# Kernel optimization log

Measured on AMD Instinct MI355X. Metric: run time of the kernel, lower is better.

Reference implementation:

```python
import jax, jax.numpy as jnp
import numpy as np

H_HEADS = 8
DIM_HEAD = 64


def setup_inputs() -> dict:
    key = jax.random.key(0)
    ks = jax.random.split(key, 5)
    b, c, Hs, Ws = 16, 32, 128, 128
    qd = H_HEADS * c              # 256 (heads*c = Linear in_features)
    inner = H_HEADS * DIM_HEAD    # 512
    s = 0.02                      # keep logits in a sane range
    return {
        "x": jax.random.normal(ks[0], (b, c, Hs, Ws), jnp.float32),
        "Wq": jax.random.normal(ks[1], (inner, qd), jnp.float32) * s,
        "Wkv": jax.random.normal(ks[2], (2 * inner, qd), jnp.float32) * s,
        "Wout": jax.random.normal(ks[3], (qd, inner), jnp.float32) * s,
        "bout": jax.random.normal(ks[4], (qd,), jnp.float32) * s,
    }


def _proj(arg, W, bias=None):
    # apply_operator_or_ffn for nn.Linear:
    # rearrange '(b h) n d -> b d (h n)', Linear over last dim, then 'b d n -> b n d'
    B, n, d = arg.shape
    bp = B // H_HEADS
    t = arg.reshape(bp, H_HEADS, n, d)
    t = jnp.transpose(t, (0, 3, 1, 2)).reshape(bp, d, H_HEADS * n)  # [b', d, h*n]
    y = t @ W.T
    if bias is not None:
        y = y + bias
    return jnp.transpose(y, (0, 2, 1))  # [b', out_features, d]


def _split_heads(t):
    # 'b (h d) n -> (b h) d n'
    bp, hd, n = t.shape
    return t.reshape(bp, H_HEADS, hd // H_HEADS, n).reshape(bp * H_HEADS, hd // H_HEADS, n)


def reference(x, Wq, Wkv, Wout, bout):
    b, c = x.shape[0], x.shape[1]
    spatial = x.shape[2:]
    N = int(np.prod(spatial))
    scale = DIM_HEAD ** -0.5
    xf = x.reshape(b, c, N)
    q = _proj(xf, Wq)              # [b/h, inner, N]
    kv = _proj(xf, Wkv)            # [b/h, 2*inner, N]
    inner = q.shape[1]
    k, v = kv[:, :inner], kv[:, inner:]
    qh, kh, vh = _split_heads(q), _split_heads(k), _split_heads(v)  # [b, DIM_HEAD, N]
    sim = jnp.einsum('bin,bjn->bij', qh, kh) * scale                 # [b, dh, dh]
    attn = jax.nn.softmax(sim, axis=-1)
    out = jnp.einsum('bnj,bjd->bnd', attn, vh)                       # [b, dh, N]
    out = _proj(out, Wout, bout)                                     # [b/h, h*c, N]
    return out.reshape(b, c, *spatial)
```

## Files before the change

### kernel.cpp

```cpp
#include <hip/hip_runtime.h>
#include <cstdint>
#include <cstddef>

using u16 = unsigned short;
using u32 = unsigned int;

typedef __attribute__((ext_vector_type(8))) short bf16x8;
typedef __attribute__((ext_vector_type(16))) float f32x16;

__device__ __forceinline__ u16 f2bf(float f) {
  union { float f; u32 i; } x; x.f = f;
  u32 r = (x.i + 0x7FFFu + ((x.i >> 16) & 1u)) >> 16;
  return (u16)r;
}
__device__ __forceinline__ bf16x8 ldbf16x8(const u16* p) {
  union { uint4 u; bf16x8 v; } t;
  t.u = *(const uint4*)p;
  return t.v;
}

constexpr int NP = 16384;


constexpr size_t OFF_C   = 0;
constexpr size_t OFF_T   = 131072;
constexpr size_t OFF_AT  = 393216;
constexpr size_t OFF_WE  = 458752;
constexpr size_t OFF_MT  = 720896;
constexpr size_t OFF_MA  = 851968;
constexpr size_t OFF_XB  = 917504;
constexpr size_t OFF_XBT = 5111808;
constexpr size_t OFF_CP1 = 9306112;
constexpr size_t NEED1   = (OFF_CP1 + 4194304) * 4;
constexpr size_t OFF_CP2 = 851968;
constexpr size_t NEED2   = (OFF_CP2 + 6291456) * 4;

__global__ __launch_bounds__(256)
void k0_cvt(const float* __restrict__ x, u16* __restrict__ XbF,
            u16* __restrict__ XbTF) {
  __shared__ u32 Fs[256 * 33];
  const int pc = blockIdx.x;
  const int g  = blockIdx.y;
  const int p0 = pc * 64;
  const float* __restrict__ Xg = x + (size_t)g * 256 * NP;
  u16* __restrict__ XbFg  = XbF  + (size_t)g * 256 * NP;
  u16* __restrict__ XbTFg = XbTF + (size_t)g * NP * 256;
  const int tid = threadIdx.x;
  const int f8i = tid & 7, rb = tid >> 3;
  const int sA = pc * 4 + (f8i >> 1);
  const int hA = f8i & 1;
  for (int pass = 0; pass < 8; ++pass) {
    const int row = rb + pass * 32;
    const size_t e0 = (size_t)row * NP + p0 + f8i * 8;
    float4 a = *(const float4*)(Xg + e0);
    float4 b = *(const float4*)(Xg + e0 + 4);
    const float v[8] = {a.x, a.y, a.z, a.w, b.x, b.y, b.z, b.w};
    uint4 s;
    s.x = (u32)f2bf(v[0]) | ((u32)f2bf(v[1]) << 16);
    s.y = (u32)f2bf(v[2]) | ((u32)f2bf(v[3]) << 16);
    s.z = (u32)f2bf(v[4]) | ((u32)f2bf(v[5]) << 16);
    s.w = (u32)f2bf(v[6]) | ((u32)f2bf(v[7]) << 16);
    const int panel = row >> 5, lc = row & 31;
    *(uint4*)(XbFg + (size_t)panel * 524288 + sA * 512 + hA * 256 + lc * 8) = s;
    u32* d = &Fs[row * 33 + f8i * 4];
    d[0] = s.x; d[1] = s.y; d[2] = s.z; d[3] = s.w;
  }
  __syncthreads();
  const int p = tid & 63, grp = tid >> 6;
  const int pp = p0 + p;
  const int panelT = pp >> 5, lcT = pp & 31;
  const u16* __restrict__ Fs16 = (const u16*)Fs;
  u16* dstT = XbTFg + (size_t)panelT * 8192 + lcT * 8;
  for (int c = 0; c < 4; ++c) {
    const int sT = grp * 4 + c;
    u32 w[8];
#pragma unroll
    for (int q = 0; q < 8; ++q) {
      const int f = grp * 64 + c * 16 + q * 2;
      u32 lo = Fs16[f * 66 + p];
      u32 hi = Fs16[(f + 1) * 66 + p];
      w[q] = lo | (hi << 16);
    }
    uint4 s0 = {w[0], w[1], w[2], w[3]};
    uint4 s1 = {w[4], w[5], w[6], w[7]};
    *(uint4*)(dstT + sT * 512)       = s0;
    *(uint4*)(dstT + sT * 512 + 256) = s1;
  }
}

__global__ __launch_bounds__(256)
void k1_mfma(const u16* __restrict__ XbF, float* __restrict__ Cpart) {
  const int tp = blockIdx.x;
  const int kc = blockIdx.y;
  const int g  = blockIdx.z;
  const int ti = tp >> 1, tj = tp & 1;
  const int tid = threadIdx.x;
  const int w = tid >> 6, half = (tid >> 5) & 1, lc = tid & 31;
  const int qi = w >> 1, qj = w & 1;
  const u16* __restrict__ Xg = XbF + (size_t)g * 256 * NP;
  const size_t koff = (size_t)kc * 16384 + half * 256 + lc * 8;
  const u16* A0 = Xg + (size_t)(ti * 4 + qi * 2 + 0) * 524288 + koff;
  const u16* A1 = Xg + (size_t)(ti * 4 + qi * 2 + 1) * 524288 + koff;
  const u16* B0 = Xg + (size_t)(tj * 4 + qj * 2 + 0) * 524288 + koff;
  const u16* B1 = Xg + (size_t)(tj * 4 + qj * 2 + 1) * 524288 + koff;
  f32x16 acc00, acc01, acc10, acc11;
#pragma unroll
  for (int i = 0; i < 16; ++i) {
    acc00[i] = 0.f; acc01[i] = 0.f; acc10[i] = 0.f; acc11[i] = 0.f;
  }
#pragma unroll 4
  for (int s = 0; s < 32; ++s) {
    bf16x8 a0 = ldbf16x8(A0 + s * 512);
    bf16x8 a1 = ldbf16x8(A1 + s * 512);
    bf16x8 b0 = ldbf16x8(B0 + s * 512);
    bf16x8 b1 = ldbf16x8(B1 + s * 512);
    acc00 = __builtin_amdgcn_mfma_f32_32x32x16_bf16(a0, b0, acc00, 0, 0, 0);
    acc01 = __builtin_amdgcn_mfma_f32_32x32x16_bf16(a0, b1, acc01, 0, 0, 0);
    acc10 = __builtin_amdgcn_mfma_f32_32x32x16_bf16(a1, b0, acc10, 0, 0, 0);
    acc11 = __builtin_amdgcn_mfma_f32_32x32x16_bf16(a1, b1, acc11, 0, 0, 0);
  }
  float* __restrict__ P = Cpart + (((size_t)g * 4 + tp) * 32 + kc) * 16384;
#pragma unroll
  for (int r = 0; r < 16; ++r) {
    const int rr = (r & 3) + 8 * (r >> 2) + 4 * half;
    const int row0 = qi * 64 + rr, col0 = qj * 64 + lc;
    P[(row0 +  0) * 128 + col0 +  0] = acc00[r];
    P[(row0 +  0) * 128 + col0 + 32] = acc01[r];
    P[(row0 + 32) * 128 + col0 +  0] = acc10[r];
    P[(row0 + 32) * 128 + col0 + 32] = acc11[r];
  }
}

__global__ __launch_bounds__(256)
void k1b_red(const float* __restrict__ Cpart, float* __restrict__ Cmat) {
  const int sl = blockIdx.x;
  const int tp = blockIdx.y;
  const int g  = blockIdx.z;
  const int ele = sl * 256 + threadIdx.x;
  const float* __restrict__ P =
      Cpart + (((size_t)g * 4 + tp) * 32) * 16384 + ele;
  float v = 0.f;
#pragma unroll
  for (int kc = 0; kc < 32; ++kc) v += P[(size_t)kc * 16384];
  const int ti = tp >> 1, tj = tp & 1;
  const int i = ele >> 7, j = ele & 127;
  Cmat[(size_t)g * 65536 + (size_t)(ti * 128 + i) * 256 + tj * 128 + j] = v;
}

__global__ __launch_bounds__(256)
void k1_gram(const float* __restrict__ x, float* __restrict__ Cpart) {
  __shared__ float As[32 * 132];
  __shared__ float Bs[32 * 132];
  const int kc = blockIdx.x, ty = blockIdx.y, g = blockIdx.z;
  const int i0 = (ty == 2) ? 128 : 0;
  const int j0 = (ty == 0) ? 0 : 128;
  const float* __restrict__ Xg = x + (size_t)g * 256 * NP;
  const int tid = threadIdx.x, lane = tid & 63, w = tid >> 6;
  const int wy = (w >> 1) * 64, wx = (w & 1) * 64;
  const int ly = (lane >> 3) * 8, lx = (lane & 7) * 8;
  float acc[8][8];
#pragma unroll
  for (int e = 0; e < 8; ++e)
#pragma unroll
    for (int f = 0; f < 8; ++f) acc[e][f] = 0.f;
  const int k8 = (tid & 3) * 8, rowb = tid >> 2, k0 = kc * 256;
  for (int s = 0; s < 8; ++s) {
    const int ks = k0 + s * 32;
#pragma unroll
    for (int pass = 0; pass < 2; ++pass) {
      const int row = rowb + pass * 64;
      const size_t ea = (size_t)(i0 + row) * NP + ks + k8;
      float4 a = *(const float4*)(Xg + ea);
      float4 b = *(const float4*)(Xg + ea + 4);
      As[(k8+0)*132+row]=a.x; As[(k8+1)*132+row]=a.y;
      As[(k8+2)*132+row]=a.z; As[(k8+3)*132+row]=a.w;
      As[(k8+4)*132+row]=b.x; As[(k8+5)*132+row]=b.y;
      As[(k8+6)*132+row]=b.z; As[(k8+7)*132+row]=b.w;
      const size_t eb = (size_t)(j0 + row) * NP + ks + k8;
      a = *(const float4*)(Xg + eb);
      b = *(const float4*)(Xg + eb + 4);
      Bs[(k8+0)*132+row]=a.x; Bs[(k8+1)*132+row]=a.y;
      Bs[(k8+2)*132+row]=a.z; Bs[(k8+3)*132+row]=a.w;
      Bs[(k8+4)*132+row]=b.x; Bs[(k8+5)*132+row]=b.y;
      Bs[(k8+6)*132+row]=b.z; Bs[(k8+7)*132+row]=b.w;
    }
    __syncthreads();
#pragma unroll 4
    for (int kk = 0; kk < 32; ++kk) {
      const float* ar = &As[kk * 132 + wy + ly];
      const float* br = &Bs[kk * 132 + wx + lx];
      float4 a0 = *(const float4*)(ar), a1 = *(const float4*)(ar + 4);
      float4 b0 = *(const float4*)(br), b1 = *(const float4*)(br + 4);
      const float av[8] = {a0.x,a0.y,a0.z,a0.w,a1.x,a1.y,a1.z,a1.w};
      const float bv[8] = {b0.x,b0.y,b0.z,b0.w,b1.x,b1.y,b1.z,b1.w};
#pragma unroll
      for (int e = 0; e < 8; ++e)
#pragma unroll
        for (int f = 0; f < 8; ++f) acc[e][f] += av[e] * bv[f];
    }
    __syncthreads();
  }
  float* __restrict__ P = Cpart + (((size_t)g * 3 + ty) * 64 + kc) * 16384;
#pragma unroll
  for (int e = 0; e < 8; ++e) {
    float* pr = P + (size_t)(wy + ly + e) * 128 + wx + lx;
    float4 s0 = {acc[e][0], acc[e][1], acc[e][2], acc[e][3]};
    float4 s1 = {acc[e][4], acc[e][5], acc[e][6], acc[e][7]};
    *(float4*)(pr)     = s0;
    *(float4*)(pr + 4) = s1;
  }
}

__global__ __launch_bounds__(256)
void k1b_reduce(const float* __restrict__ Cpart, float* __restrict__ Cmat) {
  const int sl = blockIdx.x, ty = blockIdx.y, g = blockIdx.z;
  const int ele = sl * 256 + threadIdx.x;
  const float* __restrict__ P =
      Cpart + (((size_t)g * 3 + ty) * 64) * 16384 + ele;
  float v = 0.f;
#pragma unroll 8
  for (int kc = 0; kc < 64; ++kc) v += P[(size_t)kc * 16384];
  const int i0 = (ty == 2) ? 128 : 0;
  const int j0 = (ty == 0) ? 0 : 128;
  const int i = ele >> 7, j = ele & 127;
  float* Cg = Cmat + (size_t)g * 65536;
  Cg[(size_t)(i0 + i) * 256 + (j0 + j)] = v;
  if (ty == 1) Cg[(size_t)(j0 + j) * 256 + (i0 + i)] = v;
}

__global__ __launch_bounds__(256)
void k1_gram_atomic(const float* __restrict__ x, float* __restrict__ Cmat) {
  __shared__ float As[32 * 132];
  __shared__ float Bs[32 * 132];
  const int kc = blockIdx.x, ty = blockIdx.y, g = blockIdx.z;
  const int i0 = (ty == 2) ? 128 : 0;
  const int j0 = (ty == 0) ? 0 : 128;
  const float* __restrict__ Xg = x + (size_t)g * 256 * NP;
  const int tid = threadIdx.x, lane = tid & 63, w = tid >> 6;
  const int wy = (w >> 1) * 64, wx = (w & 1) * 64;
  const int ly = (lane >> 3) * 8, lx = (lane & 7) * 8;
  float acc[8][8];
#pragma unroll
  for (int e = 0; e < 8; ++e)
#pragma unroll
    for (int f = 0; f < 8; ++f) acc[e][f] = 0.f;
  const int k8 = (tid & 3) * 8, rowb = tid >> 2, k0 = kc * 256;
  for (int s = 0; s < 8; ++s) {
    const int ks = k0 + s * 32;
#pragma unroll
    for (int pass = 0; pass < 2; ++pass) {
      const int row = rowb + pass * 64;
      const size_t ea = (size_t)(i0 + row) * NP + ks + k8;
      float4 a = *(const float4*)(Xg + ea);
      float4 b = *(const float4*)(Xg + ea + 4);
      As[(k8+0)*132+row]=a.x; As[(k8+1)*132+row]=a.y;
      As[(k8+2)*132+row]=a.z; As[(k8+3)*132+row]=a.w;
      As[(k8+4)*132+row]=b.x; As[(k8+5)*132+row]=b.y;
      As[(k8+6)*132+row]=b.z; As[(k8+7)*132+row]=b.w;
      const size_t eb = (size_t)(j0 + row) * NP + ks + k8;
      a = *(const float4*)(Xg + eb);
      b = *(const float4*)(Xg + eb + 4);
      Bs[(k8+0)*132+row]=a.x; Bs[(k8+1)*132+row]=a.y;
      Bs[(k8+2)*132+row]=a.z; Bs[(k8+3)*132+row]=a.w;
      Bs[(k8+4)*132+row]=b.x; Bs[(k8+5)*132+row]=b.y;
      Bs[(k8+6)*132+row]=b.z; Bs[(k8+7)*132+row]=b.w;
    }
    __syncthreads();
#pragma unroll 4
    for (int kk = 0; kk < 32; ++kk) {
      const float* ar = &As[kk * 132 + wy + ly];
      const float* br = &Bs[kk * 132 + wx + lx];
      float4 a0 = *(const float4*)(ar), a1 = *(const float4*)(ar + 4);
      float4 b0 = *(const float4*)(br), b1 = *(const float4*)(br + 4);
      const float av[8] = {a0.x,a0.y,a0.z,a0.w,a1.x,a1.y,a1.z,a1.w};
      const float bv[8] = {b0.x,b0.y,b0.z,b0.w,b1.x,b1.y,b1.z,b1.w};
#pragma unroll
      for (int e = 0; e < 8; ++e)
#pragma unroll
        for (int f = 0; f < 8; ++f) acc[e][f] += av[e] * bv[f];
    }
    __syncthreads();
  }
  float* Cg = Cmat + (size_t)g * 65536;
#pragma unroll
  for (int e = 0; e < 8; ++e)
#pragma unroll
    for (int f = 0; f < 8; ++f) {
      atomicAdd(&Cg[(i0+wy+ly+e)*256 + (j0+wx+lx+f)], acc[e][f]);
      if (ty == 1)
        atomicAdd(&Cg[(j0+wx+lx+f)*256 + (i0+wy+ly+e)], acc[e][f]);
    }
}

__global__ __launch_bounds__(256)
void kA_attn(const float* __restrict__ Wq, const float* __restrict__ Wkv,
             const float* __restrict__ Cmat, float* __restrict__ attn) {
  __shared__ float WqL[4 * 256];
  __shared__ float Ts[4 * 256];
  const int bh = blockIdx.x;
  const int ic = blockIdx.y;
  const int g = bh >> 3, hh = bh & 7;
  const int tid = threadIdx.x;
  const float* __restrict__ Cg = Cmat + (size_t)g * 65536;
  {
    const int r = tid >> 6, c4 = (tid & 63) * 4;
    *(float4*)(&WqL[r * 256 + c4]) =
        *(const float4*)(Wq + (size_t)(hh * 64 + ic * 4 + r) * 256 + c4);
  }
  __syncthreads();
  float acc[4] = {0.f, 0.f, 0.f, 0.f};
#pragma unroll 8
  for (int b = 0; b < 256; ++b) {
    const float cv = Cg[(size_t)b * 256 + tid];
#pragma unroll
    for (int r = 0; r < 4; ++r) acc[r] += WqL[r * 256 + b] * cv;
  }
#pragma unroll
  for (int r = 0; r < 4; ++r) Ts[r * 256 + tid] = acc[r];
  __syncthreads();
  const int r = tid >> 6, j = tid & 63;
  const float* __restrict__ Wk = Wkv + (size_t)(hh * 64 + j) * 256;
  float s = 0.f;
#pragma unroll 4
  for (int a4 = 0; a4 < 64; ++a4) {
    float4 w = *(const float4*)(Wk + a4 * 4);
    const float* t4 = &Ts[r * 256 + a4 * 4];
    s += t4[0] * w.x + t4[1] * w.y + t4[2] * w.z + t4[3] * w.w;
  }
  s *= 0.125f;
  float m = s;
#pragma unroll
  for (int off = 32; off; off >>= 1) m = fmaxf(m, __shfl_xor(m, off));
  const float e = __expf(s - m);
  float sum = e;
#pragma unroll
  for (int off = 32; off; off >>= 1) sum += __shfl_xor(sum, off);
  attn[((size_t)bh * 64 + ic * 4 + r) * 64 + j] = e / sum;
}

__global__ __launch_bounds__(256)
void kB_m(const float* __restrict__ Wout, const float* __restrict__ Wkv,
          const float* __restrict__ attn, float* __restrict__ Mp) {
  __shared__ float AtL[64 * 64];
  __shared__ float WoL[16 * 64];
  __shared__ float UL[16 * 64];
  const int bh = blockIdx.x;
  const int cc = blockIdx.y;
  const int g = bh >> 3, hh = bh & 7;
  const int tid = threadIdx.x;
  {
    const float* __restrict__ A = attn + (size_t)bh * 4096;
#pragma unroll
    for (int q = 0; q < 4; ++q)
      *(float4*)(&AtL[q * 1024 + tid * 4]) =
          *(const float4*)(A + q * 1024 + tid * 4);
  }
  {
    const int co_l = tid >> 4, i4 = (tid & 15) * 4;
    *(float4*)(&WoL[co_l * 64 + i4]) =
        *(const float4*)(Wout + (size_t)(cc * 16 + co_l) * 512 + hh * 64 + i4);
  }
  __syncthreads();
  const int j = tid & 63, cw = tid >> 6;
  float u4[4] = {0.f, 0.f, 0.f, 0.f};
#pragma unroll 4
  for (int i = 0; i < 64; ++i) {
    const float av = AtL[i * 64 + j];
#pragma unroll
    for (int u = 0; u < 4; ++u) u4[u] += WoL[(cw * 4 + u) * 64 + i] * av;
  }
  __syncthreads();
#pragma unroll
  for (int u = 0; u < 4; ++u) UL[(cw * 4 + u) * 64 + j] = u4[u];
  __syncthreads();
  float acc[16];
#pragma unroll
  for (int c = 0; c < 16; ++c) acc[c] = 0.f;
#pragma unroll 4
  for (int j2 = 0; j2 < 64; ++j2) {
    const float wv = Wkv[(size_t)(512 + hh * 64 + j2) * 256 + tid];
#pragma unroll
    for (int c = 0; c < 16; ++c) acc[c] += UL[c * 64 + j2] * wv;
  }
  float* __restrict__ P =
      Mp + (((size_t)g * 8 + hh) * 256 + cc * 16) * 256 + tid;
#pragma unroll
  for (int c = 0; c < 16; ++c) P[(size_t)c * 256] = acc[c];
}

__global__ __launch_bounds__(256)
void kC_red(const float* __restrict__ Mp, u16* __restrict__ MA) {
  const int panel = blockIdx.x >> 2;
  const int q     = blockIdx.x & 3;
  const int g     = blockIdx.y;
  const int tid = threadIdx.x;
  const float* __restrict__ Pg = Mp + (size_t)g * 8 * 65536;
  u16* __restrict__ Mg = MA + (size_t)g * 65536;
  const int item = tid + q * 256;
  const int lc = item & 31;
  const int co = panel * 32 + lc;
  const int b0 = (item >> 5) * 8;
  float v[8] = {0.f, 0.f, 0.f, 0.f, 0.f, 0.f, 0.f, 0.f};
#pragma unroll
  for (int hd = 0; hd < 8; ++hd) {
    const float* p = Pg + (size_t)hd * 65536 + (size_t)co * 256 + b0;
    float4 a = *(const float4*)(p);
    float4 b = *(const float4*)(p + 4);
    v[0] += a.x; v[1] += a.y; v[2] += a.z; v[3] += a.w;
    v[4] += b.x; v[5] += b.y; v[6] += b.z; v[7] += b.w;
  }
  uint4 sdat;
  sdat.x = (u32)f2bf(v[0]) | ((u32)f2bf(v[1]) << 16);
  sdat.y = (u32)f2bf(v[2]) | ((u32)f2bf(v[3]) << 16);
  sdat.z = (u32)f2bf(v[4]) | ((u32)f2bf(v[5]) << 16);
  sdat.w = (u32)f2bf(v[6]) | ((u32)f2bf(v[7]) << 16);
  *(uint4*)(Mg + (size_t)panel * 8192 + (size_t)item * 8) = sdat;
}

__global__ __launch_bounds__(256) void k2_T(const float* __restrict__ Wq,
                                            const float* __restrict__ Cmat,
                                            float* __restrict__ T) {
  const int bh = blockIdx.x;
  const int ic = blockIdx.y;
  const int g = bh >> 3, hh = bh & 7;
  const int tid = threadIdx.x;
  const float* __restrict__ Cg = Cmat + (size_t)g * 65536;
  const int r0 = hh * 64 + ic * 4;
  float acc[4] = {0.f, 0.f, 0.f, 0.f};
#pragma unroll 8
  for (int b = 0; b < 256; ++b) {
    const float cv = Cg[(size_t)b * 256 + tid];
#pragma unroll
    for (int ii = 0; ii < 4; ++ii)
      acc[ii] += Wq[(size_t)(r0 + ii) * 256 + b] * cv;
  }
#pragma unroll
  for (int ii = 0; ii < 4; ++ii)
    T[((size_t)bh * 64 + ic * 4 + ii) * 256 + tid] = acc[ii];
}

__global__ __launch_bounds__(256) void k3_sim(const float* __restrict__ Wkv,
                                              const float* __restrict__ T,
                                              float* __restrict__ simattn) {
  __shared__ float Ts[64 * 256];
  const int bh = blockIdx.x;
  const int jc = blockIdx.y;
  const int hh = bh & 7;
  const int tid = threadIdx.x;
  {
    const int f4i = tid & 63;
    const int rwb = tid >> 6;
    for (int pass = 0; pass < 16; ++pass) {
      const int row = rwb + pass * 4;
      float4 v = *(const float4*)(T + ((size_t)bh * 64 + row) * 256 + f4i * 4);
      const int a0 = f4i * 4;
      const float vv[4] = {v.x, v.y, v.z, v.w};
#pragma unroll
      for (int e = 0; e < 4; ++e) {
        const int a = a0 + e;
        Ts[row * 256 + (a & ~31) + ((a + row) & 31)] = vv[e];
      }
    }
  }
  __syncthreads();
  const int i  = tid & 63;
  const int jq = tid >> 6;
  const int jb = jc * 16 + jq * 4;
  float acc[4] = {0.f, 0.f, 0.f, 0.f};
#pragma unroll 4
  for (int a = 0; a < 256; ++a) {
    const float tv = Ts[i * 256 + (a & ~31) + ((a + i) & 31)];
#pragma unroll
    for (int jj = 0; jj < 4; ++jj)
      acc[jj] += Wkv[(size_t)(hh * 64 + jb + jj) * 256 + a] * tv;
  }
#pragma unroll
  for (int jj = 0; jj < 4; ++jj)
    simattn[((size_t)bh * 64 + i) * 64 + jb + jj] = acc[jj] * 0.125f;
}

__global__ __launch_bounds__(64) void k3b_softmax(float* __restrict__ simattn) {
  const int bh = blockIdx.x;
  const int i  = threadIdx.x;
  float* row = simattn + ((size_t)bh * 64 + i) * 64;
  float v[64];
  float m = -1e30f;
#pragma unroll
  for (int j = 0; j < 64; ++j) { v[j] = row[j]; m = fmaxf(m, v[j]); }
  float s = 0.f;
#pragma unroll
  for (int j = 0; j < 64; ++j) { v[j] = __expf(v[j] - m); s += v[j]; }
  const float inv = 1.0f / s;
#pragma unroll
  for (int j = 0; j < 64; ++j) row[j] = v[j] * inv;
}

__global__ __launch_bounds__(256) void k4_we(const float* __restrict__ Wout,
                                             const float* __restrict__ attn,
                                             float* __restrict__ WeT) {
  __shared__ float WL[256 * 64];
  const int jc = blockIdx.x;
  const int hh = blockIdx.y;
  const int g  = blockIdx.z;
  const int bh = g * 8 + hh;
  const int tid = threadIdx.x;
  {
    const int f4i = tid & 15;
    const int cb  = tid >> 4;
    for (int pass = 0; pass < 16; ++pass) {
      const int co = cb + pass * 16;
      float4 v = *(const float4*)(Wout + (size_t)co * 512 + hh * 64 + f4i * 4);
      const int a0 = f4i * 4;
      const float vv[4] = {v.x, v.y, v.z, v.w};
#pragma unroll
      for (int e = 0; e < 4; ++e)
        WL[co * 64 + ((a0 + e + co) & 63)] = vv[e];
    }
  }
  __syncthreads();
  const int jb = jc * 8;
  float acc[8] = {0.f, 0.f, 0.f, 0.f, 0.f, 0.f, 0.f, 0.f};
#pragma unroll 4
  for (int i = 0; i < 64; ++i) {
    const float wv = WL[tid * 64 + ((i + tid) & 63)];
#pragma unroll
    for (int je = 0; je < 8; ++je)
      acc[je] += attn[((size_t)bh * 64 + i) * 64 + jb + je] * wv;
  }
#pragma unroll
  for (int je = 0; je < 8; ++je)
    WeT[(size_t)g * 131072 + (size_t)(hh * 64 + jb + je) * 256 + tid] =
        acc[je];
}

__global__ __launch_bounds__(256)
void k5a_part(const float* __restrict__ Wkv, const float* __restrict__ WeT,
              float* __restrict__ Mp) {
  const int bc = blockIdx.x;
  const int oc = blockIdx.y;
  const int g  = blockIdx.z;
  const int tid = threadIdx.x;
  const int b0 = bc * 4;
  const float* __restrict__ Weg = WeT + (size_t)g * 131072;
  float acc[4] = {0.f, 0.f, 0.f, 0.f};
#pragma unroll 8
  for (int u = 0; u < 32; ++u) {
    const int o = oc * 32 + u;
    const float wv = Weg[(size_t)o * 256 + tid];
    const float* __restrict__ vr = Wkv + (size_t)(512 + o) * 256 + b0;
    acc[0] += vr[0] * wv;
    acc[1] += vr[1] * wv;
    acc[2] += vr[2] * wv;
    acc[3] += vr[3] * wv;
  }
#pragma unroll
  for (int be = 0; be < 4; ++be)
    Mp[(((size_t)g * 16 + oc) * 256 + b0 + be) * 256 + tid] = acc[be];
}

__global__ __launch_bounds__(256)
void k5b_red(const float* __restrict__ Mp, float* __restrict__ Mt,
             u16* __restrict__ MA) {
  const int b = blockIdx.x;
  const int g = blockIdx.y;
  const int tid = threadIdx.x;
  const float* __restrict__ P =
      Mp + ((size_t)g * 16 * 256 + b) * 256 + tid;
  float v = 0.f;
#pragma unroll
  for (int oc = 0; oc < 16; ++oc) v += P[(size_t)oc * 65536];
  Mt[(size_t)g * 65536 + (size_t)b * 256 + tid] = v;
  MA[(size_t)g * 65536 + (size_t)tid * 256 + b] = f2bf(v);
}

__global__ __launch_bounds__(256) void k5_serial(const float* __restrict__ Wkv,
                                                 const float* __restrict__ WeT,
                                                 float* __restrict__ Mt,
                                                 u16* __restrict__ MA) {
  const int bc = blockIdx.x;
  const int g  = blockIdx.y;
  const int tid = threadIdx.x;
  const int b0 = bc * 4;
  const float* __restrict__ Weg = WeT + (size_t)g * 131072;
  float acc[4] = {0.f, 0.f, 0.f, 0.f};
#pragma unroll 4
  for (int o = 0; o < 512; ++o) {
    const float wv = Weg[(size_t)o * 256 + tid];
    const float* __restrict__ vr = Wkv + (size_t)(512 + o) * 256 + b0;
    acc[0] += vr[0] * wv;
    acc[1] += vr[1] * wv;
    acc[2] += vr[2] * wv;
    acc[3] += vr[3] * wv;
  }
#pragma unroll
  for (int be = 0; be < 4; ++be) {
    Mt[(size_t)g * 65536 + (size_t)(b0 + be) * 256 + tid] = acc[be];
    MA[(size_t)g * 65536 + (size_t)tid * 256 + b0 + be] = f2bf(acc[be]);
  }
}

__global__ __launch_bounds__(256)
void k6_mfma(const u16* __restrict__ XbTF, const u16* __restrict__ MA,
             const float* __restrict__ bout, float* __restrict__ out) {
  const int pb = blockIdx.x;
  const int cb = blockIdx.y;
  const int g  = blockIdx.z;
  const int tid = threadIdx.x;
  const int w = tid >> 6, half = (tid >> 5) & 1, lc = tid & 31;
  const int p0  = pb * 128 + w * 32;
  const int co0 = cb * 128;
  const u16* __restrict__ Ap = XbTF + (size_t)g * NP * 256 +
                               (size_t)(pb * 4 + w) * 8192 + half * 256 +
                               lc * 8;
  const u16* __restrict__ Bp = MA + (size_t)g * 65536 +
                               (size_t)cb * 32768 + half * 256 + lc * 8;
  f32x16 acc[4];
#pragma unroll
  for (int t = 0; t < 4; ++t)
#pragma unroll
    for (int i = 0; i < 16; ++i) acc[t][i] = 0.f;
#pragma unroll 2
  for (int s = 0; s < 16; ++s) {
    bf16x8 a = ldbf16x8(Ap + s * 512);
#pragma unroll
    for (int t = 0; t < 4; ++t) {
      bf16x8 b = ldbf16x8(Bp + (size_t)t * 8192 + s * 512);
      acc[t] = __builtin_amdgcn_mfma_f32_32x32x16_bf16(a, b, acc[t], 0, 0, 0);
    }
  }
#pragma unroll
  for (int t = 0; t < 4; ++t) {
    const int co = co0 + t * 32 + lc;
    const float bo = bout[co];
    float* __restrict__ ocol =
        out + ((size_t)(g * 256 + co)) * NP + p0 + 4 * half;
#pragma unroll
    for (int rg = 0; rg < 4; ++rg) {
      float4 v = {acc[t][rg * 4 + 0] + bo, acc[t][rg * 4 + 1] + bo,
                  acc[t][rg * 4 + 2] + bo, acc[t][rg * 4 + 3] + bo};
      *(float4*)(ocol + rg * 8) = v;
    }
  }
}

__global__ __launch_bounds__(256)
void k6_apply(const float* __restrict__ x, const float* __restrict__ Mt,
              const float* __restrict__ bout, float* __restrict__ out) {
  __shared__ float As[32 * 132];
  __shared__ float Bs[32 * 132];
  const int pc = blockIdx.x;
  const int oy = blockIdx.y;
  const int g  = blockIdx.z;
  const int p0 = pc * 128;
  const int o0 = oy * 128;
  const float* __restrict__ Xg = x + (size_t)g * 256 * NP;
  const float* __restrict__ Mg = Mt + (size_t)g * 65536;
  const int tid  = threadIdx.x;
  const int lane = tid & 63;
  const int w    = tid >> 6;
  const int wy = (w >> 1) * 64;
  const int wx = (w & 1) * 64;
  const int ly = (lane >> 3) * 8;
  const int lx = (lane & 7) * 8;
  float acc[8][8];
#pragma unroll
  for (int e = 0; e < 8; ++e)
#pragma unroll
    for (int f = 0; f < 8; ++f) acc[e][f] = 0.f;
  const int c4 = (tid & 31) * 4;
  const int kb = tid >> 5;
  for (int s = 0; s < 8; ++s) {
#pragma unroll
    for (int r = 0; r < 4; ++r) {
      const int kk = kb + r * 8;
      const int f  = s * 32 + kk;
      *(float4*)&As[kk * 132 + c4] =
          *(const float4*)(Mg + (size_t)f * 256 + o0 + c4);
      *(float4*)&Bs[kk * 132 + c4] =
          *(const float4*)(Xg + (size_t)f * NP + p0 + c4);
    }
    __syncthreads();
#pragma unroll 4
    for (int kk = 0; kk < 32; ++kk) {
      const float* __restrict__ ar = &As[kk * 132 + wy + ly];
      const float* __restrict__ br = &Bs[kk * 132 + wx + lx];
      float4 a0 = *(const float4*)(ar);
      float4 a1 = *(const float4*)(ar + 4);
      float4 b0 = *(const float4*)(br);
      float4 b1 = *(const float4*)(br + 4);
      const float av[8] = {a0.x, a0.y, a0.z, a0.w, a1.x, a1.y, a1.z, a1.w};
      const float bv[8] = {b0.x, b0.y, b0.z, b0.w, b1.x, b1.y, b1.z, b1.w};
#pragma unroll
      for (int e = 0; e < 8; ++e)
#pragma unroll
        for (int f = 0; f < 8; ++f) acc[e][f] += av[e] * bv[f];
    }
    __syncthreads();
  }
#pragma unroll
  for (int e = 0; e < 8; ++e) {
    const int co = o0 + wy + ly + e;
    const float bo = bout[co];
    float* __restrict__ orow =
        out + ((size_t)(g * 256 + co)) * NP + p0 + wx + lx;
    float4 s0 = {acc[e][0] + bo, acc[e][1] + bo, acc[e][2] + bo,
                 acc[e][3] + bo};
    float4 s1 = {acc[e][4] + bo, acc[e][5] + bo, acc[e][6] + bo,
                 acc[e][7] + bo};
    *(float4*)(orow)     = s0;
    *(float4*)(orow + 4) = s1;
  }
}

extern "C" void kernel_launch(void* const* d_in, const int* in_sizes, int n_in,
                              void* d_out, int out_size, void* d_ws,
                              size_t ws_size, hipStream_t stream) {
  const float* x    = (const float*)d_in[0];
  const float* Wq   = (const float*)d_in[1];
  const float* Wkv  = (const float*)d_in[2];
  const float* Wout = (const float*)d_in[3];
  const float* bout = (const float*)d_in[4];
  float* out = (float*)d_out;
  float* ws  = (float*)d_ws;

  float* C    = ws + OFF_C;
  float* T    = ws + OFF_T;
  float* att  = ws + OFF_AT;
  float* WeT  = ws + OFF_WE;
  float* Mt   = ws + OFF_MT;
  u16*   MA   = (u16*)(ws + OFF_MA);
  u16*   Xb   = (u16*)(ws + OFF_XB);
  u16*   XbT  = (u16*)(ws + OFF_XBT);
  float* Cp1  = ws + OFF_CP1;
  float* Cp2  = ws + OFF_CP2;

  const bool mfma_path = (ws_size >= NEED1);
  const bool splitk    = (ws_size >= NEED2);

  if (mfma_path) {
    k0_cvt<<<dim3(256, 2), 256, 0, stream>>>(x, Xb, XbT);
    k1_mfma<<<dim3(4, 32, 2), 256, 0, stream>>>(Xb, Cp1);
    k1b_red<<<dim3(64, 4, 2), 256, 0, stream>>>(Cp1, C);
    kA_attn<<<dim3(16, 16), 256, 0, stream>>>(Wq, Wkv, C, att);
    kB_m<<<dim3(16, 16), 256, 0, stream>>>(Wout, Wkv, att, Cp1);
    kC_red<<<dim3(32, 2), 256, 0, stream>>>(Cp1, MA);
    k6_mfma<<<dim3(128, 2, 2), 256, 0, stream>>>(XbT, MA, bout, out);
    return;
  }

  if (splitk) {
    k1_gram<<<dim3(64, 3, 2), 256, 0, stream>>>(x, Cp2);
    k1b_reduce<<<dim3(64, 3, 2), 256, 0, stream>>>(Cp2, C);
  } else {
    hipMemsetAsync(C, 0, 131072 * sizeof(float), stream);
    k1_gram_atomic<<<dim3(64, 3, 2), 256, 0, stream>>>(x, C);
  }
  k2_T<<<dim3(16, 16), 256, 0, stream>>>(Wq, C, T);
  k3_sim<<<dim3(16, 4), 256, 0, stream>>>(Wkv, T, att);
  k3b_softmax<<<dim3(16), 64, 0, stream>>>(att);
  k4_we<<<dim3(8, 8, 2), 256, 0, stream>>>(Wout, att, WeT);
  if (splitk) {
    k5a_part<<<dim3(64, 16, 2), 256, 0, stream>>>(Wkv, WeT, Cp2);
    k5b_red<<<dim3(256, 2), 256, 0, stream>>>(Cp2, Mt, MA);
  } else {
    k5_serial<<<dim3(64, 2), 256, 0, stream>>>(Wkv, WeT, Mt, MA);
  }
  k6_apply<<<dim3(128, 2, 2), 256, 0, stream>>>(x, Mt, bout, out);
}
```

Before: 159.3 us.

## Drop transposed bf16 copy of x and fuse M build with its reduction

```diff
diff --git a/kernel.cpp b/kernel.cpp
--- a/kernel.cpp
+++ b/kernel.cpp
@@ -29,62 +29,35 @@
 constexpr size_t OFF_MT  = 720896;
 constexpr size_t OFF_MA  = 851968;
 constexpr size_t OFF_XB  = 917504;
-constexpr size_t OFF_XBT = 5111808;
-constexpr size_t OFF_CP1 = 9306112;
+constexpr size_t OFF_CP1 = 5111808;
 constexpr size_t NEED1   = (OFF_CP1 + 4194304) * 4;
 constexpr size_t OFF_CP2 = 851968;
 constexpr size_t NEED2   = (OFF_CP2 + 6291456) * 4;
 
 __global__ __launch_bounds__(256)
-void k0_cvt(const float* __restrict__ x, u16* __restrict__ XbF,
-            u16* __restrict__ XbTF) {
-  __shared__ u32 Fs[256 * 33];
+void k0_cvt(const float* __restrict__ x, u16* __restrict__ XbF) {
   const int pc = blockIdx.x;
   const int g  = blockIdx.y;
   const int p0 = pc * 64;
   const float* __restrict__ Xg = x + (size_t)g * 256 * NP;
-  u16* __restrict__ XbFg  = XbF  + (size_t)g * 256 * NP;
-  u16* __restrict__ XbTFg = XbTF + (size_t)g * NP * 256;
+  u16* __restrict__ XbFg = XbF + (size_t)g * 256 * NP;
   const int tid = threadIdx.x;
   const int f8i = tid & 7, rb = tid >> 3;
   const int sA = pc * 4 + (f8i >> 1);
   const int hA = f8i & 1;
+#pragma unroll
   for (int pass = 0; pass < 8; ++pass) {
     const int row = rb + pass * 32;
     const size_t e0 = (size_t)row * NP + p0 + f8i * 8;
     float4 a = *(const float4*)(Xg + e0);
     float4 b = *(const float4*)(Xg + e0 + 4);
-    const float v[8] = {a.x, a.y, a.z, a.w, b.x, b.y, b.z, b.w};
     uint4 s;
-    s.x = (u32)f2bf(v[0]) | ((u32)f2bf(v[1]) << 16);
-    s.y = (u32)f2bf(v[2]) | ((u32)f2bf(v[3]) << 16);
-    s.z = (u32)f2bf(v[4]) | ((u32)f2bf(v[5]) << 16);
-    s.w = (u32)f2bf(v[6]) | ((u32)f2bf(v[7]) << 16);
+    s.x = (u32)f2bf(a.x) | ((u32)f2bf(a.y) << 16);
+    s.y = (u32)f2bf(a.z) | ((u32)f2bf(a.w) << 16);
+    s.z = (u32)f2bf(b.x) | ((u32)f2bf(b.y) << 16);
+    s.w = (u32)f2bf(b.z) | ((u32)f2bf(b.w) << 16);
     const int panel = row >> 5, lc = row & 31;
     *(uint4*)(XbFg + (size_t)panel * 524288 + sA * 512 + hA * 256 + lc * 8) = s;
-    u32* d = &Fs[row * 33 + f8i * 4];
-    d[0] = s.x; d[1] = s.y; d[2] = s.z; d[3] = s.w;
-  }
-  __syncthreads();
-  const int p = tid & 63, grp = tid >> 6;
-  const int pp = p0 + p;
-  const int panelT = pp >> 5, lcT = pp & 31;
-  const u16* __restrict__ Fs16 = (const u16*)Fs;
-  u16* dstT = XbTFg + (size_t)panelT * 8192 + lcT * 8;
-  for (int c = 0; c < 4; ++c) {
-    const int sT = grp * 4 + c;
-    u32 w[8];
-#pragma unroll
-    for (int q = 0; q < 8; ++q) {
-      const int f = grp * 64 + c * 16 + q * 2;
-      u32 lo = Fs16[f * 66 + p];
-      u32 hi = Fs16[(f + 1) * 66 + p];
-      w[q] = lo | (hi << 16);
-    }
-    uint4 s0 = {w[0], w[1], w[2], w[3]};
-    uint4 s1 = {w[4], w[5], w[6], w[7]};
-    *(uint4*)(dstT + sT * 512)       = s0;
-    *(uint4*)(dstT + sT * 512 + 256) = s1;
   }
 }
 
@@ -145,6 +118,179 @@
   const int ti = tp >> 1, tj = tp & 1;
   const int i = ele >> 7, j = ele & 127;
   Cmat[(size_t)g * 65536 + (size_t)(ti * 128 + i) * 256 + tj * 128 + j] = v;
+}
+
+__global__ __launch_bounds__(256)
+void kA_attn(const float* __restrict__ Wq, const float* __restrict__ Wkv,
+             const float* __restrict__ Cmat, float* __restrict__ attn) {
+  __shared__ float WqL[4 * 256];
+  __shared__ float Ts[4 * 256];
+  const int bh = blockIdx.x;
+  const int ic = blockIdx.y;
+  const int g = bh >> 3, hh = bh & 7;
+  const int tid = threadIdx.x;
+  const float* __restrict__ Cg = Cmat + (size_t)g * 65536;
+  {
+    const int r = tid >> 6, c4 = (tid & 63) * 4;
+    *(float4*)(&WqL[r * 256 + c4]) =
+        *(const float4*)(Wq + (size_t)(hh * 64 + ic * 4 + r) * 256 + c4);
+  }
+  __syncthreads();
+  float acc[4] = {0.f, 0.f, 0.f, 0.f};
+#pragma unroll 8
+  for (int b = 0; b < 256; ++b) {
+    const float cv = Cg[(size_t)b * 256 + tid];
+#pragma unroll
+    for (int r = 0; r < 4; ++r) acc[r] += WqL[r * 256 + b] * cv;
+  }
+#pragma unroll
+  for (int r = 0; r < 4; ++r) Ts[r * 256 + tid] = acc[r];
+  __syncthreads();
+  const int r = tid >> 6, j = tid & 63;
+  const float* __restrict__ Wk = Wkv + (size_t)(hh * 64 + j) * 256;
+  float s = 0.f;
+#pragma unroll 4
+  for (int a4 = 0; a4 < 64; ++a4) {
+    float4 w = *(const float4*)(Wk + a4 * 4);
+    const float* t4 = &Ts[r * 256 + a4 * 4];
+    s += t4[0] * w.x + t4[1] * w.y + t4[2] * w.z + t4[3] * w.w;
+  }
+  s *= 0.125f;
+  float m = s;
+#pragma unroll
+  for (int off = 32; off; off >>= 1) m = fmaxf(m, __shfl_xor(m, off));
+  const float e = __expf(s - m);
+  float sum = e;
+#pragma unroll
+  for (int off = 32; off; off >>= 1) sum += __shfl_xor(sum, off);
+  attn[((size_t)bh * 64 + ic * 4 + r) * 64 + j] = e / sum;
+}
+
+__global__ __launch_bounds__(256)
+void kBC_m(const float* __restrict__ Wout, const float* __restrict__ Wkv,
+           const float* __restrict__ attn, u16* __restrict__ MA) {
+  __shared__ float AtL[64 * 64];
+  __shared__ float WoL[8 * 64];
+  __shared__ float UL[8 * 64];
+  __shared__ float ML[8 * 257];
+  const int cc = blockIdx.x;
+  const int g  = blockIdx.y;
+  const int tid = threadIdx.x;
+  const int j = tid & 63, cw = tid >> 6;
+  float acc[8];
+#pragma unroll
+  for (int c = 0; c < 8; ++c) acc[c] = 0.f;
+  for (int hh = 0; hh < 8; ++hh) {
+    const int bh = g * 8 + hh;
+    {
+      const float* __restrict__ A = attn + (size_t)bh * 4096;
+#pragma unroll
+      for (int q = 0; q < 4; ++q)
+        *(float4*)(&AtL[q * 1024 + tid * 4]) =
+            *(const float4*)(A + q * 1024 + tid * 4);
+    }
+    if (tid < 128) {
+      const int co_l = tid >> 4, i4 = (tid & 15) * 4;
+      *(float4*)(&WoL[co_l * 64 + i4]) = *(const float4*)(
+          Wout + (size_t)(cc * 8 + co_l) * 512 + hh * 64 + i4);
+    }
+    __syncthreads();
+    float u2[2] = {0.f, 0.f};
+#pragma unroll 4
+    for (int i = 0; i < 64; ++i) {
+      const float av = AtL[i * 64 + j];
+      u2[0] += WoL[(cw * 2 + 0) * 64 + i] * av;
+      u2[1] += WoL[(cw * 2 + 1) * 64 + i] * av;
+    }
+    __syncthreads();
+    UL[(cw * 2 + 0) * 64 + j] = u2[0];
+    UL[(cw * 2 + 1) * 64 + j] = u2[1];
+    __syncthreads();
+#pragma unroll 4
+    for (int j2 = 0; j2 < 64; ++j2) {
+      const float wv = Wkv[(size_t)(512 + hh * 64 + j2) * 256 + tid];
+#pragma unroll
+      for (int c = 0; c < 8; ++c) acc[c] += UL[c * 64 + j2] * wv;
+    }
+    __syncthreads();
+  }
+#pragma unroll
+  for (int c = 0; c < 8; ++c) ML[c * 257 + tid] = acc[c];
+  __syncthreads();
+  u16* __restrict__ Mg = MA + (size_t)g * 65536;
+  const int co_l = tid >> 5;
+  const int ib   = tid & 31;
+  const int b0 = ib * 8;
+  const int s = b0 >> 4, h = (b0 >> 3) & 1;
+  const int co = cc * 8 + co_l;
+  const int panel = co >> 5, lc = co & 31;
+  const float* mr = &ML[co_l * 257 + b0];
+  uint4 sdat;
+  sdat.x = (u32)f2bf(mr[0]) | ((u32)f2bf(mr[1]) << 16);
+  sdat.y = (u32)f2bf(mr[2]) | ((u32)f2bf(mr[3]) << 16);
+  sdat.z = (u32)f2bf(mr[4]) | ((u32)f2bf(mr[5]) << 16);
+  sdat.w = (u32)f2bf(mr[6]) | ((u32)f2bf(mr[7]) << 16);
+  *(uint4*)(Mg + (size_t)panel * 8192 + s * 512 + h * 256 + lc * 8) = sdat;
+}
+
+__global__ __launch_bounds__(256)
+void k6_mfma(const u16* __restrict__ XbF, const u16* __restrict__ MA,
+             const float* __restrict__ bout, float* __restrict__ out) {
+  __shared__ u16 T[128 * 264];
+  const int pb = blockIdx.x;
+  const int cb = blockIdx.y;
+  const int g  = blockIdx.z;
+  const int tid = threadIdx.x;
+  const u16* __restrict__ Xg = XbF + (size_t)g * 256 * NP;
+  for (int it = 0; it < 16; ++it) {
+    const int idx = it * 256 + tid;
+    const int pa  = idx >> 9;
+    const int o2  = (idx & 511) * 8;
+    union { uint4 u; u16 e[8]; } v;
+    v.u = *(const uint4*)(Xg + (size_t)pa * 524288 + (size_t)pb * 4096 + o2);
+    const int sp_l = o2 >> 9;
+    const int r    = o2 & 511;
+    const int h    = r >> 8;
+    const int lcf  = (r >> 3) & 31;
+    const int f    = pa * 32 + lcf;
+    const int pl   = sp_l * 16 + h * 8;
+#pragma unroll
+    for (int jj = 0; jj < 8; ++jj) T[(pl + jj) * 264 + f] = v.e[jj];
+  }
+  __syncthreads();
+  const int w = tid >> 6, half = (tid >> 5) & 1, lc = tid & 31;
+  const int p0  = pb * 128 + w * 32;
+  const int co0 = cb * 128;
+  const u16* __restrict__ Ap = &T[(w * 32 + lc) * 264 + half * 8];
+  const u16* __restrict__ Bp = MA + (size_t)g * 65536 +
+                               (size_t)cb * 32768 + half * 256 + lc * 8;
+  f32x16 acc[4];
+#pragma unroll
+  for (int t = 0; t < 4; ++t)
+#pragma unroll
+    for (int i = 0; i < 16; ++i) acc[t][i] = 0.f;
+#pragma unroll 2
+  for (int s = 0; s < 16; ++s) {
+    bf16x8 a = ldbf16x8(Ap + s * 16);
+#pragma unroll
+    for (int t = 0; t < 4; ++t) {
+      bf16x8 b = ldbf16x8(Bp + (size_t)t * 8192 + s * 512);
+      acc[t] = __builtin_amdgcn_mfma_f32_32x32x16_bf16(a, b, acc[t], 0, 0, 0);
+    }
+  }
+#pragma unroll
+  for (int t = 0; t < 4; ++t) {
+    const int co = co0 + t * 32 + lc;
+    const float bo = bout[co];
+    float* __restrict__ ocol =
+        out + ((size_t)(g * 256 + co)) * NP + p0 + 4 * half;
+#pragma unroll
+    for (int rg = 0; rg < 4; ++rg) {
+      float4 v = {acc[t][rg * 4 + 0] + bo, acc[t][rg * 4 + 1] + bo,
+                  acc[t][rg * 4 + 2] + bo, acc[t][rg * 4 + 3] + bo};
+      *(float4*)(ocol + rg * 8) = v;
+    }
+  }
 }
 
 __global__ __launch_bounds__(256)
@@ -292,131 +438,6 @@
     }
 }
 
-__global__ __launch_bounds__(256)
-void kA_attn(const float* __restrict__ Wq, const float* __restrict__ Wkv,
-             const float* __restrict__ Cmat, float* __restrict__ attn) {
-  __shared__ float WqL[4 * 256];
-  __shared__ float Ts[4 * 256];
-  const int bh = blockIdx.x;
-  const int ic = blockIdx.y;
-  const int g = bh >> 3, hh = bh & 7;
-  const int tid = threadIdx.x;
-  const float* __restrict__ Cg = Cmat + (size_t)g * 65536;
-  {
-    const int r = tid >> 6, c4 = (tid & 63) * 4;
-    *(float4*)(&WqL[r * 256 + c4]) =
-        *(const float4*)(Wq + (size_t)(hh * 64 + ic * 4 + r) * 256 + c4);
-  }
-  __syncthreads();
-  float acc[4] = {0.f, 0.f, 0.f, 0.f};
-#pragma unroll 8
-  for (int b = 0; b < 256; ++b) {
-    const float cv = Cg[(size_t)b * 256 + tid];
-#pragma unroll
-    for (int r = 0; r < 4; ++r) acc[r] += WqL[r * 256 + b] * cv;
-  }
-#pragma unroll
-  for (int r = 0; r < 4; ++r) Ts[r * 256 + tid] = acc[r];
-  __syncthreads();
-  const int r = tid >> 6, j = tid & 63;
-  const float* __restrict__ Wk = Wkv + (size_t)(hh * 64 + j) * 256;
-  float s = 0.f;
-#pragma unroll 4
-  for (int a4 = 0; a4 < 64; ++a4) {
-    float4 w = *(const float4*)(Wk + a4 * 4);
-    const float* t4 = &Ts[r * 256 + a4 * 4];
-    s += t4[0] * w.x + t4[1] * w.y + t4[2] * w.z + t4[3] * w.w;
-  }
-  s *= 0.125f;
-  float m = s;
-#pragma unroll
-  for (int off = 32; off; off >>= 1) m = fmaxf(m, __shfl_xor(m, off));
-  const float e = __expf(s - m);
-  float sum = e;
-#pragma unroll
-  for (int off = 32; off; off >>= 1) sum += __shfl_xor(sum, off);
-  attn[((size_t)bh * 64 + ic * 4 + r) * 64 + j] = e / sum;
-}
-
-__global__ __launch_bounds__(256)
-void kB_m(const float* __restrict__ Wout, const float* __restrict__ Wkv,
-          const float* __restrict__ attn, float* __restrict__ Mp) {
-  __shared__ float AtL[64 * 64];
-  __shared__ float WoL[16 * 64];
-  __shared__ float UL[16 * 64];
-  const int bh = blockIdx.x;
-  const int cc = blockIdx.y;
-  const int g = bh >> 3, hh = bh & 7;
-  const int tid = threadIdx.x;
-  {
-    const float* __restrict__ A = attn + (size_t)bh * 4096;
-#pragma unroll
-    for (int q = 0; q < 4; ++q)
-      *(float4*)(&AtL[q * 1024 + tid * 4]) =
-          *(const float4*)(A + q * 1024 + tid * 4);
-  }
-  {
-    const int co_l = tid >> 4, i4 = (tid & 15) * 4;
-    *(float4*)(&WoL[co_l * 64 + i4]) =
-        *(const float4*)(Wout + (size_t)(cc * 16 + co_l) * 512 + hh * 64 + i4);
-  }
-  __syncthreads();
-  const int j = tid & 63, cw = tid >> 6;
-  float u4[4] = {0.f, 0.f, 0.f, 0.f};
-#pragma unroll 4
-  for (int i = 0; i < 64; ++i) {
-    const float av = AtL[i * 64 + j];
-#pragma unroll
-    for (int u = 0; u < 4; ++u) u4[u] += WoL[(cw * 4 + u) * 64 + i] * av;
-  }
-  __syncthreads();
-#pragma unroll
-  for (int u = 0; u < 4; ++u) UL[(cw * 4 + u) * 64 + j] = u4[u];
-  __syncthreads();
-  float acc[16];
-#pragma unroll
-  for (int c = 0; c < 16; ++c) acc[c] = 0.f;
-#pragma unroll 4
-  for (int j2 = 0; j2 < 64; ++j2) {
-    const float wv = Wkv[(size_t)(512 + hh * 64 + j2) * 256 + tid];
-#pragma unroll
-    for (int c = 0; c < 16; ++c) acc[c] += UL[c * 64 + j2] * wv;
-  }
-  float* __restrict__ P =
-      Mp + (((size_t)g * 8 + hh) * 256 + cc * 16) * 256 + tid;
-#pragma unroll
-  for (int c = 0; c < 16; ++c) P[(size_t)c * 256] = acc[c];
-}
-
-__global__ __launch_bounds__(256)
-void kC_red(const float* __restrict__ Mp, u16* __restrict__ MA) {
-  const int panel = blockIdx.x >> 2;
-  const int q     = blockIdx.x & 3;
-  const int g     = blockIdx.y;
-  const int tid = threadIdx.x;
-  const float* __restrict__ Pg = Mp + (size_t)g * 8 * 65536;
-  u16* __restrict__ Mg = MA + (size_t)g * 65536;
-  const int item = tid + q * 256;
-  const int lc = item & 31;
-  const int co = panel * 32 + lc;
-  const int b0 = (item >> 5) * 8;
-  float v[8] = {0.f, 0.f, 0.f, 0.f, 0.f, 0.f, 0.f, 0.f};
-#pragma unroll
-  for (int hd = 0; hd < 8; ++hd) {
-    const float* p = Pg + (size_t)hd * 65536 + (size_t)co * 256 + b0;
-    float4 a = *(const float4*)(p);
-    float4 b = *(const float4*)(p + 4);
-    v[0] += a.x; v[1] += a.y; v[2] += a.z; v[3] += a.w;
-    v[4] += b.x; v[5] += b.y; v[6] += b.z; v[7] += b.w;
-  }
-  uint4 sdat;
-  sdat.x = (u32)f2bf(v[0]) | ((u32)f2bf(v[1]) << 16);
-  sdat.y = (u32)f2bf(v[2]) | ((u32)f2bf(v[3]) << 16);
-  sdat.z = (u32)f2bf(v[4]) | ((u32)f2bf(v[5]) << 16);
-  sdat.w = (u32)f2bf(v[6]) | ((u32)f2bf(v[7]) << 16);
-  *(uint4*)(Mg + (size_t)panel * 8192 + (size_t)item * 8) = sdat;
-}
-
 __global__ __launch_bounds__(256) void k2_T(const float* __restrict__ Wq,
                                             const float* __restrict__ Cmat,
                                             float* __restrict__ T) {
@@ -596,50 +617,6 @@
   for (int be = 0; be < 4; ++be) {
     Mt[(size_t)g * 65536 + (size_t)(b0 + be) * 256 + tid] = acc[be];
     MA[(size_t)g * 65536 + (size_t)tid * 256 + b0 + be] = f2bf(acc[be]);
-  }
-}
-
-__global__ __launch_bounds__(256)
-void k6_mfma(const u16* __restrict__ XbTF, const u16* __restrict__ MA,
-             const float* __restrict__ bout, float* __restrict__ out) {
-  const int pb = blockIdx.x;
-  const int cb = blockIdx.y;
-  const int g  = blockIdx.z;
-  const int tid = threadIdx.x;
-  const int w = tid >> 6, half = (tid >> 5) & 1, lc = tid & 31;
-  const int p0  = pb * 128 + w * 32;
-  const int co0 = cb * 128;
-  const u16* __restrict__ Ap = XbTF + (size_t)g * NP * 256 +
-                               (size_t)(pb * 4 + w) * 8192 + half * 256 +
-                               lc * 8;
-  const u16* __restrict__ Bp = MA + (size_t)g * 65536 +
-                               (size_t)cb * 32768 + half * 256 + lc * 8;
-  f32x16 acc[4];
-#pragma unroll
-  for (int t = 0; t < 4; ++t)
-#pragma unroll
-    for (int i = 0; i < 16; ++i) acc[t][i] = 0.f;
-#pragma unroll 2
-  for (int s = 0; s < 16; ++s) {
-    bf16x8 a = ldbf16x8(Ap + s * 512);
-#pragma unroll
-    for (int t = 0; t < 4; ++t) {
-      bf16x8 b = ldbf16x8(Bp + (size_t)t * 8192 + s * 512);
-      acc[t] = __builtin_amdgcn_mfma_f32_32x32x16_bf16(a, b, acc[t], 0, 0, 0);
-    }
-  }
-#pragma unroll
-  for (int t = 0; t < 4; ++t) {
-    const int co = co0 + t * 32 + lc;
-    const float bo = bout[co];
-    float* __restrict__ ocol =
-        out + ((size_t)(g * 256 + co)) * NP + p0 + 4 * half;
-#pragma unroll
-    for (int rg = 0; rg < 4; ++rg) {
-      float4 v = {acc[t][rg * 4 + 0] + bo, acc[t][rg * 4 + 1] + bo,
-                  acc[t][rg * 4 + 2] + bo, acc[t][rg * 4 + 3] + bo};
-      *(float4*)(ocol + rg * 8) = v;
-    }
   }
 }
 
@@ -730,7 +707,6 @@
   float* Mt   = ws + OFF_MT;
   u16*   MA   = (u16*)(ws + OFF_MA);
   u16*   Xb   = (u16*)(ws + OFF_XB);
-  u16*   XbT  = (u16*)(ws + OFF_XBT);
   float* Cp1  = ws + OFF_CP1;
   float* Cp2  = ws + OFF_CP2;
 
@@ -738,13 +714,12 @@
   const bool splitk    = (ws_size >= NEED2);
 
   if (mfma_path) {
-    k0_cvt<<<dim3(256, 2), 256, 0, stream>>>(x, Xb, XbT);
+    k0_cvt<<<dim3(256, 2), 256, 0, stream>>>(x, Xb);
     k1_mfma<<<dim3(4, 32, 2), 256, 0, stream>>>(Xb, Cp1);
     k1b_red<<<dim3(64, 4, 2), 256, 0, stream>>>(Cp1, C);
     kA_attn<<<dim3(16, 16), 256, 0, stream>>>(Wq, Wkv, C, att);
-    kB_m<<<dim3(16, 16), 256, 0, stream>>>(Wout, Wkv, att, Cp1);
-    kC_red<<<dim3(32, 2), 256, 0, stream>>>(Cp1, MA);
-    k6_mfma<<<dim3(128, 2, 2), 256, 0, stream>>>(XbT, MA, bout, out);
+    kBC_m<<<dim3(32, 2), 256, 0, stream>>>(Wout, Wkv, att, MA);
+    k6_mfma<<<dim3(128, 2, 2), 256, 0, stream>>>(Xb, MA, bout, out);
     return;
   }
 
```

After: 194.4 us. 22.1% more time.
